# Kernel optimization log

Measured on AMD Instinct MI355X. Metric: run time of the kernel, lower is better.

The kernel has to match this reference:

```python
import jax, jax.numpy as jnp
import numpy as np


def _ste(q, x):
    # straight-through estimator: forward = q, gradient = identity w.r.t. x
    return x + jax.lax.stop_gradient(q - x)


def quant_w(w, bit_w=8):
    # symmetric per-tensor weight quantization fused into QConv2d
    qmax = 2.0 ** (bit_w - 1) - 1.0
    scale = jnp.max(jnp.abs(w)) / qmax
    q = jnp.clip(jnp.round(w / scale), -qmax, qmax) * scale
    return _ste(q, w)


def quant_a(x, bit_a=8):
    # unsigned activation quantizer: clamp to [0,1], uniform bit_a levels
    n = 2.0 ** bit_a - 1.0
    xc = jnp.clip(x, 0.0, 1.0)
    q = jnp.round(xc * n) / n
    return _ste(q, xc)


def exp_norm2d(x, gamma, beta, eps=1e-5):
    # instance-style norm: per (N, C) statistics over spatial dims, affine
    mean = jnp.mean(x, axis=(2, 3), keepdims=True)
    var = jnp.var(x, axis=(2, 3), keepdims=True)
    xn = (x - mean) * jax.lax.rsqrt(var + eps)
    return xn * gamma[None, :, None, None] + beta[None, :, None, None]


def qconv(x, w, stride, pad, bit_w=8):
    wq = quant_w(w, bit_w)
    return jax.lax.conv_general_dilated(
        x, wq, window_strides=(stride, stride),
        padding=[(pad, pad), (pad, pad)],
        dimension_numbers=('NCHW', 'OIHW', 'NCHW'))


def setup_inputs() -> dict:
    key = jax.random.key(0)
    ks = jax.random.split(key, 4)
    C_in, C_out, H = 256, 512, 56
    return {
        'x': jax.random.normal(ks[0], (32, C_in, H, H), jnp.float32),
        'w1': jax.random.normal(ks[1], (C_out, C_in, 3, 3), jnp.float32) * 0.05,
        'g1': jnp.ones((C_out,), jnp.float32),
        'b1': jnp.zeros((C_out,), jnp.float32),
        'w2': jax.random.normal(ks[2], (C_out, C_out, 3, 3), jnp.float32) * 0.05,
        'g2': jnp.ones((C_out,), jnp.float32),
        'b2': jnp.zeros((C_out,), jnp.float32),
        'wp': jax.random.normal(ks[3], (C_out, C_in, 1, 1), jnp.float32) * 0.05,
        'gp': jnp.ones((C_out,), jnp.float32),
        'bp': jnp.zeros((C_out,), jnp.float32),
    }


def reference(x, w1, g1, b1, w2, g2, b2, wp, gp, bp):
    # main branch: QConv(s2) -> ExpNorm -> act quant -> QConv(s1) -> ExpNorm
    h = qconv(x, w1, stride=2, pad=1)
    h = exp_norm2d(h, g1, b1)
    h = quant_a(h, bit_a=8)
    h = qconv(h, w2, stride=1, pad=1)
    h = exp_norm2d(h, g2, b2)
    # projection shortcut: QConv 1x1 stride 2 -> ExpNorm
    s = qconv(x, wp, stride=2, pad=0)
    s = exp_norm2d(s, gp, bp)
    return h + s
```

## Files before the change

kernel.cpp:

```cpp
#include <hip/hip_runtime.h>
#include <cstdint>
#include <cstddef>


typedef unsigned short ushort_t;
typedef __attribute__((ext_vector_type(8))) short bf16x8;
typedef __attribute__((ext_vector_type(4))) float f32x4;
typedef __attribute__((ext_vector_type(4))) int i32x4;

#define NB   32
#define C_IN 256
#define HIN  56
#define CO   512
#define OHW  784
#define OWD  28
#define MTOT (NB * OHW)

constexpr size_t OFF_XH   = 0;
constexpr size_t OFF_A1   = OFF_XH  + 51380224;
constexpr size_t OFF_H2   = OFF_A1  + 25690112;
constexpr size_t OFF_S    = OFF_H2  + 51380224;
constexpr size_t OFF_WT1  = OFF_S   + 51380224;
constexpr size_t OFF_WT2  = OFF_WT1 + 2359296;
constexpr size_t OFF_WTP  = OFF_WT2 + 4718592;
constexpr size_t OFF_PSUM = OFF_WTP + 262144;
constexpr size_t OFF_A1N  = OFF_PSUM + 2097152;
constexpr size_t OFF_B1N  = OFF_A1N + 65536;
constexpr size_t OFF_A2N  = OFF_B1N + 65536;
constexpr size_t OFF_B2N  = OFF_A2N + 65536;
constexpr size_t OFF_APN  = OFF_B2N + 65536;
constexpr size_t OFF_BPN  = OFF_APN + 65536;
constexpr size_t OFF_MX   = OFF_BPN + 65536;
constexpr size_t OFF_ZB   = OFF_MX  + 16;
constexpr size_t OFF_CS   = OFF_ZB  + 2048;

__device__ __forceinline__ ushort_t f2bf(float f) {
    unsigned u = __float_as_uint(f);
    u += 0x7FFFu + ((u >> 16) & 1u);
    return (ushort_t)(u >> 16);
}
__device__ __forceinline__ float bf2f(ushort_t u) {
    return __uint_as_float(((unsigned)u) << 16);
}

__device__ __forceinline__ void async_copy16(const void* g, const void* l) {
    auto gp = (const __attribute__((address_space(1))) unsigned int*)(uintptr_t)g;
    auto lp = (__attribute__((address_space(3))) unsigned int*)(unsigned int)(uintptr_t)l;
    __builtin_amdgcn_global_load_lds(gp, lp, 16, 0, 0);
}

__global__ void to_nhwc_k(const float* __restrict__ x, ushort_t* __restrict__ xh) {
    __shared__ float tile[64][33];
    const int wt0 = blockIdx.x * 32;
    const int ct0 = blockIdx.y * 64;
    const int nh  = blockIdx.z;
    const int n = nh / HIN, h = nh - n * HIN;
    {
        const int tx = threadIdx.x & 31;
        const int ty = threadIdx.x >> 5;
        const int w  = wt0 + tx;
#pragma unroll
        for (int j = 0; j < 8; ++j) {
            int cl = ty + j * 8;
            if (w < HIN)
                tile[cl][tx] = x[(((size_t)n * C_IN + ct0 + cl) * HIN + h) * HIN + w];
        }
    }
    __syncthreads();
    {
        const int tc = threadIdx.x & 63;
        const int tw = threadIdx.x >> 6;
#pragma unroll
        for (int j = 0; j < 8; ++j) {
            int wl = tw + j * 4;
            int w  = wt0 + wl;
            if (w < HIN)
                xh[(((size_t)n * HIN + h) * HIN + w) * C_IN + ct0 + tc] =
                    f2bf(tile[tc][wl]);
        }
    }
}

__global__ void absmax3_k(const float* __restrict__ w1, int n1,
                          const float* __restrict__ w2, int n2,
                          const float* __restrict__ wp, int np,
                          unsigned* out) {
    const float* w; int nelem;
    if (blockIdx.y == 0)      { w = w1; nelem = n1; }
    else if (blockIdx.y == 1) { w = w2; nelem = n2; }
    else                      { w = wp; nelem = np; }
    int stride = gridDim.x * blockDim.x;
    float m = 0.f;
    for (int i = blockIdx.x * blockDim.x + threadIdx.x; i < nelem; i += stride)
        m = fmaxf(m, fabsf(w[i]));
#pragma unroll
    for (int off = 32; off > 0; off >>= 1)
        m = fmaxf(m, __shfl_down(m, off));
    if ((threadIdx.x & 63) == 0) atomicMax(out + blockIdx.y, __float_as_uint(m));
}

template <int CO_, int CI_, int KHW_>
__global__ void quantw_k(const float* __restrict__ w, const unsigned* __restrict__ mx,
                         ushort_t* __restrict__ wt) {
    const int total = KHW_ * CO_ * CI_;
    int idx = blockIdx.x * 256 + threadIdx.x;
    if (idx >= total) return;
    float scale = __uint_as_float(*mx) * (1.0f / 127.0f);
    float inv   = scale > 0.f ? 1.0f / scale : 0.f;
    int khw = idx / (CO_ * CI_);
    int r   = idx - khw * (CO_ * CI_);
    int co  = r / CI_;
    int ci  = r - co * CI_;
    float v  = w[((size_t)co * CI_ + ci) * KHW_ + khw];
    float qv = rintf(v * inv);
    qv = fminf(127.f, fmaxf(-127.f, qv));
    wt[idx] = f2bf(qv * scale);
}

__global__ void quantw_i8_k(const float* __restrict__ w, const unsigned* __restrict__ mx,
                            signed char* __restrict__ wt) {
    const int total = 9 * CO * CO;
    int idx = blockIdx.x * 256 + threadIdx.x;
    if (idx >= total) return;
    float scale = __uint_as_float(*mx) * (1.0f / 127.0f);
    float inv   = scale > 0.f ? 1.0f / scale : 0.f;
    int khw = idx / (CO * CO);
    int r   = idx - khw * (CO * CO);
    int co  = r / CO;
    int ci  = r - co * CO;
    float v  = w[((size_t)co * CO + ci) * 9 + khw];
    float qv = rintf(v * inv);
    qv = fminf(127.f, fmaxf(-127.f, qv));
    wt[idx] = (signed char)(int)qv;
}

__global__ void colsum_k(const signed char* __restrict__ wt, float* __restrict__ cs) {
    const int khw = blockIdx.x;
    const int co  = blockIdx.y * 32 + (threadIdx.x & 31);
    const int cig = threadIdx.x >> 5;
    const signed char* p = wt + ((size_t)khw * CO + co) * CO + cig * 64;
    int s = 0;
#pragma unroll
    for (int i = 0; i < 64; ++i) s += p[i];
    __shared__ int red[8][32];
    red[cig][threadIdx.x & 31] = s;
    __syncthreads();
    if (cig == 0) {
        int tot = 0;
#pragma unroll
        for (int g = 0; g < 8; ++g) tot += red[g][threadIdx.x & 31];
        cs[khw * CO + co] = (float)tot;
    }
}

template <int CIN, int KH, int KW, int STRIDE, int PAD, int IH, int IW>
__launch_bounds__(512, 2)
__global__ void conv8p_k(const ushort_t* __restrict__ xin,
                         const ushort_t* __restrict__ wt,
                         ushort_t* __restrict__ out,
                         const ushort_t* __restrict__ zbuf,
                         float* __restrict__ psum, float* __restrict__ pss) {
    constexpr int BK  = 64;
    constexpr int CKT = CIN / BK;
    constexpr int KT  = KH * KW * CKT;

    __shared__ alignas(16) short As[2 * 256 * BK];
    __shared__ alignas(16) short Bs[2 * 256 * BK];

    const int tid  = threadIdx.x;
    const int lane = tid & 63;
    const int wv   = tid >> 6;
    const int wm   = wv >> 2;
    const int wn   = wv & 3;
    const int lrow = lane & 15;
    const int lq   = lane >> 4;
    const int sw   = lrow & 7;

    const int bid = blockIdx.x;
    const int xcd = bid & 7;
    const int j   = bid >> 3;
    const int wg  = (xcd < 4 ? xcd * 25 : 100 + (xcd - 4) * 24) + j;
    const int m0  = (wg >> 1) * 256;
    const int co0 = (wg & 1) * 256;

    const int arow = tid >> 3;
    const int ach  = tid & 7;
    long abase[4]; unsigned amask[4]; int bco[4];
#pragma unroll
    for (int c = 0; c < 4; ++c) {
        int row = c * 64 + arow;
        int m   = m0 + row;
        int n   = m / OHW;
        int sp  = m - n * OHW;
        int oh  = sp / OWD, ow = sp - oh * OWD;
        int ihb = oh * STRIDE - PAD, iwb = ow * STRIDE - PAD;
        int swz = (ach ^ (row & 7)) * 8;
        abase[c] = ((long)n * (IH * IW) + (long)ihb * IW + iwb) * CIN + swz;
        unsigned mk = 0;
#pragma unroll
        for (int kh = 0; kh < KH; ++kh)
#pragma unroll
            for (int kw = 0; kw < KW; ++kw) {
                int ih = ihb + kh, iw = iwb + kw;
                if ((unsigned)ih < (unsigned)IH && (unsigned)iw < (unsigned)IW)
                    mk |= 1u << (kh * KW + kw);
            }
        amask[c] = mk;
        bco[c]   = (co0 + row) * CIN + swz;
    }

    auto stageA = [&](int c, int nb, long aoff, int khw) {
        const ushort_t* src = ((amask[c] >> khw) & 1)
            ? xin + (abase[c] + aoff) : zbuf;
        async_copy16(src, (const void*)&As[nb * 16384 + c * 4096 + wv * 512]);
    };
    auto stageB = [&](int c, int nb, int boff) {
        async_copy16(wt + (boff + bco[c]),
                     (const void*)&Bs[nb * 16384 + c * 4096 + wv * 512]);
    };

    f32x4 acc[8][4];
#pragma unroll
    for (int a = 0; a < 8; ++a)
#pragma unroll
        for (int b = 0; b < 4; ++b) acc[a][b] = {0.f, 0.f, 0.f, 0.f};

    stageB(0, 0, 0); stageB(1, 0, 0); stageB(2, 0, 0); stageB(3, 0, 0);
    stageA(0, 0, 0, 0); stageA(1, 0, 0, 0); stageA(2, 0, 0, 0); stageA(3, 0, 0, 0);
    asm volatile("s_waitcnt vmcnt(0)" ::: "memory");
    __builtin_amdgcn_s_barrier();

    int  khw_n = 0, kw_n = 0, ck_n = 1;
    long aoff_n = BK;
    int  boff_n = BK;

    int cur = 0;
    for (int t = 0; t < KT; ++t) {
        const bool hn = (t + 1 < KT);
        const int  nb = cur ^ 1;
        const short* Acur = &As[cur * 16384];
        const short* Bcur = &Bs[cur * 16384];

        if (hn) {
            stageB(0, nb, boff_n); stageB(1, nb, boff_n);
            stageB(2, nb, boff_n); stageB(3, nb, boff_n);
            stageA(0, nb, aoff_n, khw_n); stageA(1, nb, aoff_n, khw_n);
            stageA(2, nb, aoff_n, khw_n); stageA(3, nb, aoff_n, khw_n);
        }
        __builtin_amdgcn_sched_barrier(0);

        bf16x8 af[4][2], bfr[2][2][2];

#pragma unroll
        for (int mi = 0; mi < 4; ++mi) {
            const int row = wm * 128 + mi * 16 + lrow;
#pragma unroll
            for (int ks = 0; ks < 2; ++ks) {
                const int ch = ((ks * 4 + lq) ^ sw) * 8;
                af[mi][ks] = *(const bf16x8*)&Acur[row * BK + ch];
            }
        }
#pragma unroll
        for (int qn = 0; qn < 2; ++qn)
#pragma unroll
            for (int ni = 0; ni < 2; ++ni) {
                const int row = wn * 64 + qn * 32 + ni * 16 + lrow;
#pragma unroll
                for (int ks = 0; ks < 2; ++ks) {
                    const int ch = ((ks * 4 + lq) ^ sw) * 8;
                    bfr[qn][ni][ks] = *(const bf16x8*)&Bcur[row * BK + ch];
                }
            }
#pragma unroll
        for (int mi = 0; mi < 4; ++mi)
#pragma unroll
            for (int qn = 0; qn < 2; ++qn)
#pragma unroll
                for (int ni = 0; ni < 2; ++ni)
#pragma unroll
                    for (int ks = 0; ks < 2; ++ks)
                        acc[mi][qn * 2 + ni] =
                            __builtin_amdgcn_mfma_f32_16x16x32_bf16(
                                af[mi][ks], bfr[qn][ni][ks],
                                acc[mi][qn * 2 + ni], 0, 0, 0);

#pragma unroll
        for (int mi = 0; mi < 4; ++mi) {
            const int row = wm * 128 + 64 + mi * 16 + lrow;
#pragma unroll
            for (int ks = 0; ks < 2; ++ks) {
                const int ch = ((ks * 4 + lq) ^ sw) * 8;
                af[mi][ks] = *(const bf16x8*)&Acur[row * BK + ch];
            }
        }
#pragma unroll
        for (int mi = 0; mi < 4; ++mi)
#pragma unroll
            for (int qn = 0; qn < 2; ++qn)
#pragma unroll
                for (int ni = 0; ni < 2; ++ni)
#pragma unroll
                    for (int ks = 0; ks < 2; ++ks)
                        acc[4 + mi][qn * 2 + ni] =
                            __builtin_amdgcn_mfma_f32_16x16x32_bf16(
                                af[mi][ks], bfr[qn][ni][ks],
                                acc[4 + mi][qn * 2 + ni], 0, 0, 0);

        asm volatile("s_waitcnt vmcnt(0)" ::: "memory");
        __builtin_amdgcn_sched_barrier(0);
        __builtin_amdgcn_s_barrier();

        if (hn) {
            ck_n++;
            if (ck_n == CKT) {
                ck_n = 0; khw_n++; kw_n++;
                if (kw_n == KW) { kw_n = 0; aoff_n += (long)(IW - KW) * CIN + BK; }
                else            { aoff_n += BK; }
                boff_n += (CO - 1) * CIN + BK;
            } else {
                aoff_n += BK; boff_n += BK;
            }
        }
        cur ^= 1;
    }

    const int mb = m0 + wm * 128 + lq * 4;
    const int cb = co0 + wn * 64 + lrow;
#pragma unroll
    for (int mi = 0; mi < 8; ++mi)
#pragma unroll
        for (int ni = 0; ni < 4; ++ni)
#pragma unroll
            for (int r = 0; r < 4; ++r)
                out[(size_t)(mb + mi * 16 + r) * CO + (cb + ni * 16)] =
                    f2bf(acc[mi][ni][r]);

    const int n0 = m0 / OHW;
    const int mS = (n0 + 1) * OHW;
    float sv[2][4], qv[2][4];
#pragma unroll
    for (int g = 0; g < 2; ++g)
#pragma unroll
        for (int ni = 0; ni < 4; ++ni) { sv[g][ni] = 0.f; qv[g][ni] = 0.f; }
#pragma unroll
    for (int mi = 0; mi < 8; ++mi)
#pragma unroll
        for (int ni = 0; ni < 4; ++ni)
#pragma unroll
            for (int r = 0; r < 4; ++r) {
                float v = acc[mi][ni][r];
                int m = mb + mi * 16 + r;
                int g = (m >= mS) ? 1 : 0;
                sv[g][ni] += v; qv[g][ni] += v * v;
            }
#pragma unroll
    for (int d = 16; d <= 32; d <<= 1)
#pragma unroll
        for (int g = 0; g < 2; ++g)
#pragma unroll
            for (int ni = 0; ni < 4; ++ni) {
                sv[g][ni] += __shfl_xor(sv[g][ni], d);
                qv[g][ni] += __shfl_xor(qv[g][ni], d);
            }
    if (lq == 0) {
        const bool split = (mS < m0 + 256);
#pragma unroll
        for (int ni = 0; ni < 4; ++ni) {
            atomicAdd(&psum[n0 * CO + cb + ni * 16], sv[0][ni]);
            atomicAdd(&pss [n0 * CO + cb + ni * 16], qv[0][ni]);
            if (split) {
                atomicAdd(&psum[(n0 + 1) * CO + cb + ni * 16], sv[1][ni]);
                atomicAdd(&pss [(n0 + 1) * CO + cb + ni * 16], qv[1][ni]);
            }
        }
    }
}

__launch_bounds__(512, 2)
__global__ void conv_i8_k(const signed char* __restrict__ xin,
                          const signed char* __restrict__ wt,
                          const float* __restrict__ colsum,
                          const unsigned* __restrict__ mxp,
                          ushort_t* __restrict__ out,
                          const signed char* __restrict__ zbuf,
                          float* __restrict__ psum, float* __restrict__ pss) {
    constexpr int CIN = 512, BK = 64, CKT = 8, KT = 72;
    constexpr int IH = 28, IW = 28;

    __shared__ alignas(16) signed char As[2 * 256 * BK];
    __shared__ alignas(16) signed char Bs[2 * 256 * BK];

    const int tid  = threadIdx.x;
    const int lane = tid & 63;
    const int wv   = tid >> 6;
    const int wm   = wv >> 2;
    const int wn   = wv & 3;
    const int lrow = lane & 15;
    const int lq   = lane >> 4;

    const int bid = blockIdx.x;
    const int xcd = bid & 7;
    const int j   = bid >> 3;
    const int wg  = (xcd < 4 ? xcd * 25 : 100 + (xcd - 4) * 24) + j;
    const int m0  = (wg >> 1) * 256;
    const int co0 = (wg & 1) * 256;

    const int arow2 = tid >> 2;
    const int ach2  = tid & 3;
    long abase[2]; unsigned amask[2]; int bco[2];
#pragma unroll
    for (int c = 0; c < 2; ++c) {
        int row = c * 128 + arow2;
        int m   = m0 + row;
        int n   = m / OHW;
        int sp  = m - n * OHW;
        int oh  = sp / OWD, ow = sp - oh * OWD;
        int ihb = oh - 1, iwb = ow - 1;
        int swz = (ach2 ^ ((row >> 1) & 3)) * 16;
        abase[c] = ((long)n * (IH * IW) + (long)ihb * IW + iwb) * CIN + swz;
        unsigned mk = 0;
#pragma unroll
        for (int kh = 0; kh < 3; ++kh)
#pragma unroll
            for (int kw = 0; kw < 3; ++kw) {
                int ih = ihb + kh, iw = iwb + kw;
                if ((unsigned)ih < (unsigned)IH && (unsigned)iw < (unsigned)IW)
                    mk |= 1u << (kh * 3 + kw);
            }
        amask[c] = mk;
        bco[c]   = (co0 + row) * CIN + swz;
    }

    auto stageA = [&](int c, int nb, long aoff, int khw) {
        const signed char* src = ((amask[c] >> khw) & 1)
            ? xin + (abase[c] + aoff) : zbuf;
        async_copy16(src, (const void*)&As[nb * 16384 + c * 8192 + wv * 1024]);
    };
    auto stageB = [&](int c, int nb, int boff) {
        async_copy16(wt + (boff + bco[c]),
                     (const void*)&Bs[nb * 16384 + c * 8192 + wv * 1024]);
    };

    i32x4 acc[8][4];
#pragma unroll
    for (int a = 0; a < 8; ++a)
#pragma unroll
        for (int b = 0; b < 4; ++b) acc[a][b] = {0, 0, 0, 0};

    stageB(0, 0, 0); stageB(1, 0, 0);
    stageA(0, 0, 0, 0); stageA(1, 0, 0, 0);
    asm volatile("s_waitcnt vmcnt(0)" ::: "memory");
    __builtin_amdgcn_s_barrier();

    int  khw_n = 0, kw_n = 0, ck_n = 1;
    long aoff_n = BK;
    int  boff_n = BK;

    int cur = 0;
    for (int t = 0; t < KT; ++t) {
        const bool hn = (t + 1 < KT);
        const int  nb = cur ^ 1;
        const signed char* Acur = &As[cur * 16384];
        const signed char* Bcur = &Bs[cur * 16384];

        if (hn) {
            stageB(0, nb, boff_n); stageB(1, nb, boff_n);
            stageA(0, nb, aoff_n, khw_n); stageA(1, nb, aoff_n, khw_n);
        }
        __builtin_amdgcn_sched_barrier(0);

        i32x4 af[8], bfr[4];
#pragma unroll
        for (int mi = 0; mi < 8; ++mi) {
            const int row = wm * 128 + mi * 16 + lrow;
            af[mi] = *(const i32x4*)&Acur[row * BK + ((lq ^ ((row >> 1) & 3)) * 16)];
        }
#pragma unroll
        for (int ni = 0; ni < 4; ++ni) {
            const int row = wn * 64 + ni * 16 + lrow;
            bfr[ni] = *(const i32x4*)&Bcur[row * BK + ((lq ^ ((row >> 1) & 3)) * 16)];
        }
#pragma unroll
        for (int mi = 0; mi < 8; ++mi)
#pragma unroll
            for (int ni = 0; ni < 4; ++ni)
                acc[mi][ni] = __builtin_amdgcn_mfma_i32_16x16x64_i8(
                    af[mi], bfr[ni], acc[mi][ni], 0, 0, 0);

        asm volatile("s_waitcnt vmcnt(0)" ::: "memory");
        __builtin_amdgcn_sched_barrier(0);
        __builtin_amdgcn_s_barrier();

        if (hn) {
            ck_n++;
            if (ck_n == CKT) {
                ck_n = 0; khw_n++; kw_n++;
                if (kw_n == 3) { kw_n = 0; aoff_n += (long)(IW - 3) * CIN + BK; }
                else           { aoff_n += BK; }
                boff_n += (CO - 1) * CIN + BK;
            } else {
                aoff_n += BK; boff_n += BK;
            }
        }
        cur ^= 1;
    }

    const int mb = m0 + wm * 128 + lq * 4;
    const int cb = co0 + wn * 64 + lrow;
    const float scale = __uint_as_float(*mxp) * (1.0f / 127.0f);
    const float sc    = scale * (1.0f / 255.0f);
    const float c128  = 128.0f * sc;

    float Sall[4], Sr0[4], Sr2[4], Sc0[4], Sc2[4], K0[4], K2[4], K6[4], K8[4];
#pragma unroll
    for (int ni = 0; ni < 4; ++ni) {
        float cs[9];
#pragma unroll
        for (int k = 0; k < 9; ++k) cs[k] = colsum[k * CO + cb + ni * 16];
        Sall[ni] = cs[0]+cs[1]+cs[2]+cs[3]+cs[4]+cs[5]+cs[6]+cs[7]+cs[8];
        Sr0[ni] = cs[0]+cs[1]+cs[2];  Sr2[ni] = cs[6]+cs[7]+cs[8];
        Sc0[ni] = cs[0]+cs[3]+cs[6];  Sc2[ni] = cs[2]+cs[5]+cs[8];
        K0[ni] = cs[0]; K2[ni] = cs[2]; K6[ni] = cs[6]; K8[ni] = cs[8];
    }

    const int n0 = m0 / OHW;
    const int mS = (n0 + 1) * OHW;
    float sv[2][4], qvv[2][4];
#pragma unroll
    for (int g = 0; g < 2; ++g)
#pragma unroll
        for (int ni = 0; ni < 4; ++ni) { sv[g][ni] = 0.f; qvv[g][ni] = 0.f; }

#pragma unroll
    for (int mi = 0; mi < 8; ++mi)
#pragma unroll
        for (int r = 0; r < 4; ++r) {
            const int m  = mb + mi * 16 + r;
            const int n  = m / OHW;
            const int sp = m - n * OHW;
            const int oh = sp / OWD, ow = sp - oh * OWD;
            const int g  = (m >= mS) ? 1 : 0;
#pragma unroll
            for (int ni = 0; ni < 4; ++ni) {
                float T = Sall[ni];
                if (oh == 0)       T -= Sr0[ni];
                if (oh == OWD - 1) T -= Sr2[ni];
                if (ow == 0)       T -= Sc0[ni];
                if (ow == OWD - 1) T -= Sc2[ni];
                if (oh == 0 && ow == 0)             T += K0[ni];
                if (oh == 0 && ow == OWD - 1)       T += K2[ni];
                if (oh == OWD - 1 && ow == 0)       T += K6[ni];
                if (oh == OWD - 1 && ow == OWD - 1) T += K8[ni];
                float val = sc * (float)acc[mi][ni][r] + c128 * T;
                out[(size_t)m * CO + (cb + ni * 16)] = f2bf(val);
                sv[g][ni] += val; qvv[g][ni] += val * val;
            }
        }
#pragma unroll
    for (int d = 16; d <= 32; d <<= 1)
#pragma unroll
        for (int g = 0; g < 2; ++g)
#pragma unroll
            for (int ni = 0; ni < 4; ++ni) {
                sv[g][ni]  += __shfl_xor(sv[g][ni], d);
                qvv[g][ni] += __shfl_xor(qvv[g][ni], d);
            }
    if (lq == 0) {
        const bool split = (mS < m0 + 256);
#pragma unroll
        for (int ni = 0; ni < 4; ++ni) {
            atomicAdd(&psum[n0 * CO + cb + ni * 16], sv[0][ni]);
            atomicAdd(&pss [n0 * CO + cb + ni * 16], qvv[0][ni]);
            if (split) {
                atomicAdd(&psum[(n0 + 1) * CO + cb + ni * 16], sv[1][ni]);
                atomicAdd(&pss [(n0 + 1) * CO + cb + ni * 16], qvv[1][ni]);
            }
        }
    }
}

__global__ void statsf3_k(const float* __restrict__ ps0, const float* __restrict__ qs0,
                          const float* __restrict__ g0, const float* __restrict__ bb0,
                          float* __restrict__ ao0, float* __restrict__ bo0,
                          const float* __restrict__ ps1, const float* __restrict__ qs1,
                          const float* __restrict__ g1, const float* __restrict__ bb1,
                          float* __restrict__ ao1, float* __restrict__ bo1,
                          const float* __restrict__ ps2, const float* __restrict__ qs2,
                          const float* __restrict__ g2, const float* __restrict__ bb2,
                          float* __restrict__ ao2, float* __restrict__ bo2) {
    const float *ps, *qs, *g, *bb; float *ao, *bo;
    if (blockIdx.y == 0)      { ps = ps0; qs = qs0; g = g0; bb = bb0; ao = ao0; bo = bo0; }
    else if (blockIdx.y == 1) { ps = ps1; qs = qs1; g = g1; bb = bb1; ao = ao1; bo = bo1; }
    else                      { ps = ps2; qs = qs2; g = g2; bb = bb2; ao = ao2; bo = bo2; }
    int idx = blockIdx.x * 256 + threadIdx.x;
    int c = idx & 511;
    float s  = ps[idx];
    float ss = qs[idx];
    float mean = s * (1.0f / 784.0f);
    float var  = ss * (1.0f / 784.0f) - mean * mean;
    float rstd = rsqrtf(var + 1e-5f);
    float a = rstd * g[c];
    ao[idx] = a;
    bo[idx] = bb[c] - mean * a;
}

__global__ void norm_quant_i8_k(const ushort_t* __restrict__ h, const float* __restrict__ a_,
                                const float* __restrict__ b_, signed char* __restrict__ o) {
    int idx = blockIdx.x * 256 + threadIdx.x;
    int row = idx >> 6;
    int c0  = (idx & 63) * 8;
    int n   = row / OHW;
    bf16x8 v = ((const bf16x8*)h)[idx];
    const float* ap = a_ + n * CO + c0;
    const float* bp = b_ + n * CO + c0;
    unsigned lo = 0, hi = 0;
#pragma unroll
    for (int k = 0; k < 8; ++k) {
        float f = bf2f((ushort_t)v[k]) * ap[k] + bp[k];
        float kq = rintf(fminf(fmaxf(f, 0.f), 1.f) * 255.f);
        int s8 = (int)kq - 128;
        unsigned b = (unsigned)(s8 & 0xFF);
        if (k < 4) lo |= b << (8 * k);
        else       hi |= b << (8 * (k - 4));
    }
    ((uint2*)o)[idx] = make_uint2(lo, hi);
}

__global__ void final_k(const ushort_t* __restrict__ h2, const ushort_t* __restrict__ s,
                        const float* __restrict__ a2, const float* __restrict__ b2,
                        const float* __restrict__ ap_, const float* __restrict__ bp_,
                        float* __restrict__ out) {
    __shared__ float tile[64][33];
    const int sp0 = blockIdx.x * 32;
    const int c0  = blockIdx.y * 64;
    const int n   = blockIdx.z;
    const int tx  = threadIdx.x & 31;
    const int ty  = threadIdx.x >> 5;
#pragma unroll
    for (int j = 0; j < 4; ++j) {
        int spl = ty + j * 8;
        int sp  = sp0 + spl;
        if (sp < OHW) {
            int c = c0 + tx * 2;
            size_t ix = ((size_t)n * OHW + sp) * CO + c;
            int ci = n * CO + c;
            ushort2 vh = *(const ushort2*)&h2[ix];
            ushort2 vs = *(const ushort2*)&s[ix];
            tile[tx * 2][spl] =
                bf2f(vh.x) * a2[ci] + b2[ci] + bf2f(vs.x) * ap_[ci] + bp_[ci];
            tile[tx * 2 + 1][spl] =
                bf2f(vh.y) * a2[ci + 1] + b2[ci + 1] + bf2f(vs.y) * ap_[ci + 1] + bp_[ci + 1];
        }
    }
    __syncthreads();
    const int sp = sp0 + tx;
#pragma unroll
    for (int j = 0; j < 8; ++j) {
        int cl = ty + j * 8;
        if (sp < OHW)
            out[((size_t)n * CO + c0 + cl) * OHW + sp] = tile[cl][tx];
    }
}

extern "C" void kernel_launch(void* const* d_in, const int* in_sizes, int n_in,
                              void* d_out, int out_size, void* d_ws, size_t ws_size,
                              hipStream_t stream) {
    const float* x  = (const float*)d_in[0];
    const float* w1 = (const float*)d_in[1];
    const float* g1 = (const float*)d_in[2];
    const float* b1 = (const float*)d_in[3];
    const float* w2 = (const float*)d_in[4];
    const float* g2 = (const float*)d_in[5];
    const float* b2 = (const float*)d_in[6];
    const float* wp = (const float*)d_in[7];
    const float* gp = (const float*)d_in[8];
    const float* bp = (const float*)d_in[9];
    float* out = (float*)d_out;
    char* ws = (char*)d_ws;

    ushort_t*    xh    = (ushort_t*)(ws + OFF_XH);
    signed char* a1    = (signed char*)(ws + OFF_A1);
    ushort_t*    h2    = (ushort_t*)(ws + OFF_H2);
    ushort_t*    sbuf  = (ushort_t*)(ws + OFF_S);
    ushort_t*    wt1   = (ushort_t*)(ws + OFF_WT1);
    signed char* wt2i  = (signed char*)(ws + OFF_WT2);
    ushort_t*    wtp   = (ushort_t*)(ws + OFF_WTP);
    float*    psum1 = (float*)(ws + OFF_PSUM);
    float*    pss1  = (float*)(ws + OFF_PSUM + 65536);
    float*    psum2 = (float*)(ws + OFF_PSUM + 131072);
    float*    pss2  = (float*)(ws + OFF_PSUM + 196608);
    float*    psump = (float*)(ws + OFF_PSUM + 262144);
    float*    pssp  = (float*)(ws + OFF_PSUM + 327680);
    float*    a1n  = (float*)(ws + OFF_A1N);
    float*    b1n  = (float*)(ws + OFF_B1N);
    float*    a2n  = (float*)(ws + OFF_A2N);
    float*    b2n  = (float*)(ws + OFF_B2N);
    float*    apn  = (float*)(ws + OFF_APN);
    float*    bpn  = (float*)(ws + OFF_BPN);
    unsigned* mx   = (unsigned*)(ws + OFF_MX);
    ushort_t* zb   = (ushort_t*)(ws + OFF_ZB);
    float*    cs   = (float*)(ws + OFF_CS);
    ushort_t* h1   = (ushort_t*)out;

    hipMemsetAsync(ws + OFF_MX, 0, 16 + 2048, stream);
    hipMemsetAsync(ws + OFF_PSUM, 0, 393216, stream);

    to_nhwc_k<<<dim3(2, 4, NB * HIN), 256, 0, stream>>>(x, xh);
    absmax3_k<<<dim3(512, 3), 256, 0, stream>>>(w1, CO * C_IN * 9,
                                                w2, CO * CO * 9,
                                                wp, C_IN * CO, mx);
    quantw_k<CO, C_IN, 9><<<dim3(4608), 256, 0, stream>>>(w1, mx + 0, wt1);
    quantw_i8_k<<<dim3(9216), 256, 0, stream>>>(w2, mx + 1, wt2i);
    quantw_k<CO, C_IN, 1><<<dim3(512), 256, 0, stream>>>(wp, mx + 2, wtp);
    colsum_k<<<dim3(9, 16), 256, 0, stream>>>(wt2i, cs);

    conv8p_k<C_IN, 3, 3, 2, 1, HIN, HIN>
        <<<dim3(196), 512, 0, stream>>>(xh, wt1, h1, (const ushort_t*)zb, psum1, pss1);
    statsf3_k<<<dim3(64, 1), 256, 0, stream>>>(psum1, pss1, g1, b1, a1n, b1n,
                                               psum1, pss1, g1, b1, a1n, b1n,
                                               psum1, pss1, g1, b1, a1n, b1n);
    norm_quant_i8_k<<<dim3(MTOT * CO / 8 / 256), 256, 0, stream>>>(h1, a1n, b1n, a1);

    conv_i8_k<<<dim3(196), 512, 0, stream>>>(a1, wt2i, cs, mx + 1, h2,
                                             (const signed char*)zb, psum2, pss2);
    conv8p_k<C_IN, 1, 1, 2, 0, HIN, HIN>
        <<<dim3(196), 512, 0, stream>>>(xh, wtp, sbuf, (const ushort_t*)zb, psump, pssp);

    statsf3_k<<<dim3(64, 2), 256, 0, stream>>>(psum2, pss2, g2, b2, a2n, b2n,
                                               psump, pssp, gp, bp, apn, bpn,
                                               psum2, pss2, g2, b2, a2n, b2n);

    final_k<<<dim3(25, 8, NB), 256, 0, stream>>>(h2, sbuf, a2n, b2n, apn, bpn, out);
}
```

Before: 316.3 us.

## Load int8 conv B fragments directly from global into registers; fuse colsum into quantization

The int8 3x3 conv no longer stages weight tiles through LDS. Each lane loads its B fragments straight from global memory into registers, double-buffered across a two-step unrolled loop, while A keeps its LDS double buffer. This removes LDS traffic and shared memory for B, at the cost of more global/L2 loads and extra registers. The colsum kernel is also folded into the int8 weight quantizer using a wave shuffle reduction plus float atomics, which removes one launch; the colsum region is now cleared by the existing memset.

```diff
diff --git a/kernel.cpp b/kernel.cpp
--- a/kernel.cpp
+++ b/kernel.cpp
@@ -118,10 +118,8 @@
 }
 
 __global__ void quantw_i8_k(const float* __restrict__ w, const unsigned* __restrict__ mx,
-                            signed char* __restrict__ wt) {
-    const int total = 9 * CO * CO;
+                            signed char* __restrict__ wt, float* __restrict__ cs) {
     int idx = blockIdx.x * 256 + threadIdx.x;
-    if (idx >= total) return;
     float scale = __uint_as_float(*mx) * (1.0f / 127.0f);
     float inv   = scale > 0.f ? 1.0f / scale : 0.f;
     int khw = idx / (CO * CO);
@@ -131,26 +129,13 @@
     float v  = w[((size_t)co * CO + ci) * 9 + khw];
     float qv = rintf(v * inv);
     qv = fminf(127.f, fmaxf(-127.f, qv));
-    wt[idx] = (signed char)(int)qv;
-}
-
-__global__ void colsum_k(const signed char* __restrict__ wt, float* __restrict__ cs) {
-    const int khw = blockIdx.x;
-    const int co  = blockIdx.y * 32 + (threadIdx.x & 31);
-    const int cig = threadIdx.x >> 5;
-    const signed char* p = wt + ((size_t)khw * CO + co) * CO + cig * 64;
-    int s = 0;
-#pragma unroll
-    for (int i = 0; i < 64; ++i) s += p[i];
-    __shared__ int red[8][32];
-    red[cig][threadIdx.x & 31] = s;
-    __syncthreads();
-    if (cig == 0) {
-        int tot = 0;
-#pragma unroll
-        for (int g = 0; g < 8; ++g) tot += red[g][threadIdx.x & 31];
-        cs[khw * CO + co] = (float)tot;
-    }
+    int iq = (int)qv;
+    wt[idx] = (signed char)iq;
+    int s = iq;
+#pragma unroll
+    for (int off = 32; off > 0; off >>= 1)
+        s += __shfl_down(s, off);
+    if ((threadIdx.x & 63) == 0) atomicAdd(&cs[khw * CO + co], (float)s);
 }
 
 template <int CIN, int KH, int KW, int STRIDE, int PAD, int IH, int IW>
@@ -388,7 +373,6 @@
     constexpr int IH = 28, IW = 28;
 
     __shared__ alignas(16) signed char As[2 * 256 * BK];
-    __shared__ alignas(16) signed char Bs[2 * 256 * BK];
 
     const int tid  = threadIdx.x;
     const int lane = tid & 63;
@@ -407,7 +391,7 @@
 
     const int arow2 = tid >> 2;
     const int ach2  = tid & 3;
-    long abase[2]; unsigned amask[2]; int bco[2];
+    long abase[2]; unsigned amask[2];
 #pragma unroll
     for (int c = 0; c < 2; ++c) {
         int row = c * 128 + arow2;
@@ -428,7 +412,6 @@
                     mk |= 1u << (kh * 3 + kw);
             }
         amask[c] = mk;
-        bco[c]   = (co0 + row) * CIN + swz;
     }
 
     auto stageA = [&](int c, int nb, long aoff, int khw) {
@@ -436,10 +419,11 @@
             ? xin + (abase[c] + aoff) : zbuf;
         async_copy16(src, (const void*)&As[nb * 16384 + c * 8192 + wv * 1024]);
     };
-    auto stageB = [&](int c, int nb, int boff) {
-        async_copy16(wt + (boff + bco[c]),
-                     (const void*)&Bs[nb * 16384 + c * 8192 + wv * 1024]);
-    };
+
+    const signed char* bptr[4];
+#pragma unroll
+    for (int ni = 0; ni < 4; ++ni)
+        bptr[ni] = wt + (size_t)(co0 + wn * 64 + ni * 16 + lrow) * CIN + lq * 16;
 
     i32x4 acc[8][4];
 #pragma unroll
@@ -447,62 +431,93 @@
 #pragma unroll
         for (int b = 0; b < 4; ++b) acc[a][b] = {0, 0, 0, 0};
 
-    stageB(0, 0, 0); stageB(1, 0, 0);
+    i32x4 bfrA[4], bfrB[4];
+
     stageA(0, 0, 0, 0); stageA(1, 0, 0, 0);
+#pragma unroll
+    for (int ni = 0; ni < 4; ++ni) bfrA[ni] = *(const i32x4*)(bptr[ni]);
     asm volatile("s_waitcnt vmcnt(0)" ::: "memory");
     __builtin_amdgcn_s_barrier();
 
     int  khw_n = 0, kw_n = 0, ck_n = 1;
     long aoff_n = BK;
-    int  boff_n = BK;
 
     int cur = 0;
-    for (int t = 0; t < KT; ++t) {
-        const bool hn = (t + 1 < KT);
-        const int  nb = cur ^ 1;
-        const signed char* Acur = &As[cur * 16384];
-        const signed char* Bcur = &Bs[cur * 16384];
-
-        if (hn) {
-            stageB(0, nb, boff_n); stageB(1, nb, boff_n);
+#pragma unroll 1
+    for (int tt = 0; tt < KT / 2; ++tt) {
+        {
+            const int nb = cur ^ 1;
+            const int bo = (khw_n << 18) + ck_n * BK;
+#pragma unroll
+            for (int ni = 0; ni < 4; ++ni)
+                bfrB[ni] = *(const i32x4*)(bptr[ni] + bo);
             stageA(0, nb, aoff_n, khw_n); stageA(1, nb, aoff_n, khw_n);
-        }
-        __builtin_amdgcn_sched_barrier(0);
-
-        i32x4 af[8], bfr[4];
-#pragma unroll
-        for (int mi = 0; mi < 8; ++mi) {
-            const int row = wm * 128 + mi * 16 + lrow;
-            af[mi] = *(const i32x4*)&Acur[row * BK + ((lq ^ ((row >> 1) & 3)) * 16)];
-        }
-#pragma unroll
-        for (int ni = 0; ni < 4; ++ni) {
-            const int row = wn * 64 + ni * 16 + lrow;
-            bfr[ni] = *(const i32x4*)&Bcur[row * BK + ((lq ^ ((row >> 1) & 3)) * 16)];
-        }
-#pragma unroll
-        for (int mi = 0; mi < 8; ++mi)
-#pragma unroll
-            for (int ni = 0; ni < 4; ++ni)
-                acc[mi][ni] = __builtin_amdgcn_mfma_i32_16x16x64_i8(
-                    af[mi], bfr[ni], acc[mi][ni], 0, 0, 0);
-
-        asm volatile("s_waitcnt vmcnt(0)" ::: "memory");
-        __builtin_amdgcn_sched_barrier(0);
-        __builtin_amdgcn_s_barrier();
-
-        if (hn) {
-            ck_n++;
-            if (ck_n == CKT) {
-                ck_n = 0; khw_n++; kw_n++;
-                if (kw_n == 3) { kw_n = 0; aoff_n += (long)(IW - 3) * CIN + BK; }
-                else           { aoff_n += BK; }
-                boff_n += (CO - 1) * CIN + BK;
-            } else {
-                aoff_n += BK; boff_n += BK;
-            }
-        }
-        cur ^= 1;
+            {
+                ck_n++;
+                if (ck_n == CKT) {
+                    ck_n = 0; khw_n++; kw_n++;
+                    if (kw_n == 3) { kw_n = 0; aoff_n += (long)(IW - 3) * CIN + BK; }
+                    else           { aoff_n += BK; }
+                } else { aoff_n += BK; }
+            }
+            __builtin_amdgcn_sched_barrier(0);
+
+            const signed char* Acur = &As[cur * 16384];
+            i32x4 af[8];
+#pragma unroll
+            for (int mi = 0; mi < 8; ++mi) {
+                const int row = wm * 128 + mi * 16 + lrow;
+                af[mi] = *(const i32x4*)&Acur[row * BK + ((lq ^ ((row >> 1) & 3)) * 16)];
+            }
+#pragma unroll
+            for (int mi = 0; mi < 8; ++mi)
+#pragma unroll
+                for (int ni = 0; ni < 4; ++ni)
+                    acc[mi][ni] = __builtin_amdgcn_mfma_i32_16x16x64_i8(
+                        af[mi], bfrA[ni], acc[mi][ni], 0, 0, 0);
+
+            asm volatile("s_waitcnt vmcnt(0)" ::: "memory");
+            __builtin_amdgcn_sched_barrier(0);
+            __builtin_amdgcn_s_barrier();
+            cur ^= 1;
+        }
+        {
+            const bool hn = (2 * tt + 2 < KT);
+            const int  nb = cur ^ 1;
+            if (hn) {
+                const int bo = (khw_n << 18) + ck_n * BK;
+#pragma unroll
+                for (int ni = 0; ni < 4; ++ni)
+                    bfrA[ni] = *(const i32x4*)(bptr[ni] + bo);
+                stageA(0, nb, aoff_n, khw_n); stageA(1, nb, aoff_n, khw_n);
+                ck_n++;
+                if (ck_n == CKT) {
+                    ck_n = 0; khw_n++; kw_n++;
+                    if (kw_n == 3) { kw_n = 0; aoff_n += (long)(IW - 3) * CIN + BK; }
+                    else           { aoff_n += BK; }
+                } else { aoff_n += BK; }
+            }
+            __builtin_amdgcn_sched_barrier(0);
+
+            const signed char* Acur = &As[cur * 16384];
+            i32x4 af[8];
+#pragma unroll
+            for (int mi = 0; mi < 8; ++mi) {
+                const int row = wm * 128 + mi * 16 + lrow;
+                af[mi] = *(const i32x4*)&Acur[row * BK + ((lq ^ ((row >> 1) & 3)) * 16)];
+            }
+#pragma unroll
+            for (int mi = 0; mi < 8; ++mi)
+#pragma unroll
+                for (int ni = 0; ni < 4; ++ni)
+                    acc[mi][ni] = __builtin_amdgcn_mfma_i32_16x16x64_i8(
+                        af[mi], bfrB[ni], acc[mi][ni], 0, 0, 0);
+
+            asm volatile("s_waitcnt vmcnt(0)" ::: "memory");
+            __builtin_amdgcn_sched_barrier(0);
+            __builtin_amdgcn_s_barrier();
+            cur ^= 1;
+        }
     }
 
     const int mb = m0 + wm * 128 + lq * 4;
@@ -702,7 +717,7 @@
     float*    cs   = (float*)(ws + OFF_CS);
     ushort_t* h1   = (ushort_t*)out;
 
-    hipMemsetAsync(ws + OFF_MX, 0, 16 + 2048, stream);
+    hipMemsetAsync(ws + OFF_MX, 0, 16 + 2048 + 18432, stream);
     hipMemsetAsync(ws + OFF_PSUM, 0, 393216, stream);
 
     to_nhwc_k<<<dim3(2, 4, NB * HIN), 256, 0, stream>>>(x, xh);
@@ -710,9 +725,8 @@
                                                 w2, CO * CO * 9,
                                                 wp, C_IN * CO, mx);
     quantw_k<CO, C_IN, 9><<<dim3(4608), 256, 0, stream>>>(w1, mx + 0, wt1);
-    quantw_i8_k<<<dim3(9216), 256, 0, stream>>>(w2, mx + 1, wt2i);
+    quantw_i8_k<<<dim3(9216), 256, 0, stream>>>(w2, mx + 1, wt2i, cs);
     quantw_k<CO, C_IN, 1><<<dim3(512), 256, 0, stream>>>(wp, mx + 2, wtp);
-    colsum_k<<<dim3(9, 16), 256, 0, stream>>>(wt2i, cs);
 
     conv8p_k<C_IN, 3, 3, 2, 1, HIN, HIN>
         <<<dim3(196), 512, 0, stream>>>(xh, wt1, h1, (const ushort_t*)zb, psum1, pss1);
```

Result: slower. 364.7 us (+15.3%).
